# Optimization experiments

Hardware: AMD Instinct MI355X
Metric: run time of the kernel (lower is better)

The kernel has to match this reference:

```python
import jax, jax.numpy as jnp
import numpy as np

B, S, H, NH, P = 1, 2048, 1024, 16, 2
D = H // NH
SCALE = 1.0 / np.sqrt(D).astype(np.float32)


def _lin(x, W, b):
    # x: [..., in] @ W: [in, out] + b: [out]
    return x @ W + b


def _split_heads(x):
    # [..., S, H] -> [..., NH, S, D]
    return x.reshape(*x.shape[:-2], x.shape[-2], NH, D).swapaxes(-3, -2)


def _merge_heads(x):
    # [..., NH, S, D] -> [..., S, H]
    return x.swapaxes(-3, -2).reshape(*x.shape[:-3], x.shape[-2], H)


def setup_inputs() -> dict:
    key = jax.random.key(0)
    ks = jax.random.split(key, 20)
    w = lambda k, i, o: jax.random.normal(k, (i, o), jnp.float32) * 0.02
    inp = {
        "hidden_states": jax.random.normal(ks[0], (B, S, H), jnp.float32),
        "past_states": jax.random.normal(ks[1], (P, B, S, H), jnp.float32),
        "Wq": w(ks[2], H, H), "bq": jnp.zeros((H,), jnp.float32),
        "Wk": w(ks[3], H, H), "bk": jnp.zeros((H,), jnp.float32),
        "Wv": w(ks[4], H, H), "bv": jnp.zeros((H,), jnp.float32),
        "Wo": w(ks[5], H, H), "bo": jnp.zeros((H,), jnp.float32),
        "Wrq": w(ks[6], H, H), "brq": jnp.zeros((H,), jnp.float32),
        "Wrk": w(ks[7], H, H), "brk": jnp.zeros((H,), jnp.float32),
        "Wrv": w(ks[8], H, H), "brv": jnp.zeros((H,), jnp.float32),
        "Wg": w(ks[9], 2 * H, H), "bg": jnp.zeros((H,), jnp.float32),
    }
    return inp


def reference(hidden_states, past_states, Wq, bq, Wk, bk, Wv, bv, Wo, bo,
              Wrq, brq, Wrk, brk, Wrv, brv, Wg, bg):
    # --- standard self-attention ---
    q = _split_heads(_lin(hidden_states, Wq, bq))  # [B,NH,S,D]
    k = _split_heads(_lin(hidden_states, Wk, bk))
    v = _split_heads(_lin(hidden_states, Wv, bv))
    scores = jnp.einsum('bhsd,bhtd->bhst', q, k) * SCALE
    attn = jax.nn.softmax(scores, axis=-1)
    ctx = jnp.einsum('bhst,bhtd->bhsd', attn, v)
    output = _lin(_merge_heads(ctx), Wo, bo)  # [B,S,H]

    # --- recursive attention over past states (recursion_level > 0) ---
    rq = _split_heads(_lin(output, Wrq, brq))           # [B,NH,S,D]
    rk = _split_heads(_lin(past_states, Wrk, brk))      # [P,B,NH,S,D]
    rv = _split_heads(_lin(past_states, Wrv, brv))
    rscores = jnp.einsum('bhsd,pbhtd->pbhst', rq, rk) * SCALE
    rattn = jax.nn.softmax(rscores, axis=-1)
    rctx = jnp.einsum('pbhst,pbhtd->pbhsd', rattn, rv)
    recursive_output = _merge_heads(rctx).mean(axis=0)  # [B,S,H]

    gate = jax.nn.sigmoid(_lin(jnp.concatenate([output, recursive_output], axis=-1), Wg, bg))
    output = output * (1.0 - gate) + recursive_output * gate
    return output
```

## Files before the change

### kernel.cpp

```cpp
#include <hip/hip_runtime.h>
#include <hip/hip_bf16.h>

#define S_LEN 2048
#define HDIM  1024
#define NHEAD 16
#define DHEAD 64
#define SCALE_F 0.125f

typedef __bf16 bf16;
typedef __bf16 bf16x4 __attribute__((ext_vector_type(4)));
typedef __bf16 bf16x8 __attribute__((ext_vector_type(8)));
typedef float  f32x4  __attribute__((ext_vector_type(4)));

#define MFMA16(a,b,c) __builtin_amdgcn_mfma_f32_16x16x32_bf16((a),(b),(c),0,0,0)

__global__ void cvt_f32_bf16_kernel(const float* __restrict__ in,
                                    bf16* __restrict__ out, int n4) {
  int i = blockIdx.x * blockDim.x + threadIdx.x;
  int stride = gridDim.x * blockDim.x;
  for (; i < n4; i += stride) {
    float4 v = ((const float4*)in)[i];
    bf16x4 o = { (bf16)v.x, (bf16)v.y, (bf16)v.z, (bf16)v.w };
    ((bf16x4*)out)[i] = o;
  }
}

struct TrJob { const float* in; bf16* out; };
struct TrArgs { TrJob j[8]; };

__global__ void transp_cvt_kernel(TrArgs args, int rows, int cols) {
  TrJob t = args.j[blockIdx.z];
  __shared__ float tile[32][33];
  int tx = threadIdx.x, ty = threadIdx.y;
  int c0 = blockIdx.x * 32, r0 = blockIdx.y * 32;
  for (int j = ty; j < 32; j += 8)
    tile[j][tx] = t.in[(size_t)(r0 + j) * cols + c0 + tx];
  __syncthreads();
  for (int j = ty; j < 32; j += 8)
    t.out[(size_t)(c0 + j) * rows + r0 + tx] = (bf16)tile[tx][j];
}

__global__ void transp_head_kernel(const bf16* __restrict__ in,
                                   bf16* __restrict__ out) {
  __shared__ bf16 tile[32][33];
  int h = blockIdx.z;
  int t0 = blockIdx.x * 32, d0 = blockIdx.y * 32;
  int tx = threadIdx.x, ty = threadIdx.y;
  for (int j = ty; j < 32; j += 8)
    tile[j][tx] = in[(size_t)(t0 + j) * HDIM + h * DHEAD + d0 + tx];
  __syncthreads();
  for (int j = ty; j < 32; j += 8)
    out[((size_t)h * DHEAD + d0 + j) * S_LEN + t0 + tx] = tile[tx][j];
}

struct GemmJob { const bf16* A; const bf16* Bt; const float* bias; bf16* Cb; float* Cf; };
struct GemmArgs { GemmJob j[6]; };

__launch_bounds__(256)
__global__ void gemm_bt_kernel(GemmArgs args, int M, int N, int K) {
  GemmJob jb = args.j[blockIdx.z];
  const int bn = blockIdx.x, bm = blockIdx.y;
  const int tid = threadIdx.x;
  const int wave = tid >> 6, lane = tid & 63;
  const int wr = wave >> 1, wc = wave & 1;
  const int l16 = lane & 15, lq = lane >> 4;

  __shared__ alignas(16) bf16 As[128][40];
  __shared__ alignas(16) bf16 Bs[128][40];

  f32x4 acc[4][4];
#pragma unroll
  for (int i = 0; i < 4; ++i)
#pragma unroll
    for (int j = 0; j < 4; ++j) acc[i][j] = (f32x4){0.f, 0.f, 0.f, 0.f};

  const bf16* Ap = jb.A + (size_t)bm * 128 * K;
  const bf16* Bp = jb.Bt + (size_t)bn * 128 * K;

  for (int kt = 0; kt < K; kt += 32) {
    __syncthreads();
#pragma unroll
    for (int it = 0; it < 2; ++it) {
      int idx = tid + it * 256;
      int r = idx >> 2, c8 = (idx & 3) << 3;
      *(bf16x8*)(&As[r][c8]) = *(const bf16x8*)(Ap + (size_t)r * K + kt + c8);
      *(bf16x8*)(&Bs[r][c8]) = *(const bf16x8*)(Bp + (size_t)r * K + kt + c8);
    }
    __syncthreads();

    bf16x8 af[4], bfr[4];
#pragma unroll
    for (int i = 0; i < 4; ++i)
      af[i] = *(const bf16x8*)(&As[wr * 64 + i * 16 + l16][lq * 8]);
#pragma unroll
    for (int j = 0; j < 4; ++j)
      bfr[j] = *(const bf16x8*)(&Bs[wc * 64 + j * 16 + l16][lq * 8]);
#pragma unroll
    for (int i = 0; i < 4; ++i)
#pragma unroll
      for (int j = 0; j < 4; ++j)
        acc[i][j] = MFMA16(af[i], bfr[j], acc[i][j]);
  }

#pragma unroll
  for (int i = 0; i < 4; ++i) {
#pragma unroll
    for (int j = 0; j < 4; ++j) {
      int row0 = bm * 128 + wr * 64 + i * 16 + lq * 4;
      int col  = bn * 128 + wc * 64 + j * 16 + l16;
      float bv = jb.bias ? jb.bias[col] : 0.0f;
#pragma unroll
      for (int r = 0; r < 4; ++r) {
        float v = acc[i][j][r] + bv;
        size_t off = (size_t)(row0 + r) * N + col;
        if (jb.Cb) jb.Cb[off] = (bf16)v;
        if (jb.Cf) jb.Cf[off] = v;
      }
    }
  }
}

__launch_bounds__(256)
__global__ void flash_attn_kernel(const bf16* __restrict__ Q,
                                  const bf16* __restrict__ Kin,
                                  const bf16* __restrict__ VT,
                                  bf16* __restrict__ Ob,
                                  float* __restrict__ Of,
                                  size_t kStride, size_t vStride, size_t oStride) {
  const int qb = blockIdx.x, h = blockIdx.y, p = blockIdx.z;
  const bf16* Kp = Kin + (size_t)p * kStride;
  const bf16* Vp = VT + (size_t)p * vStride;
  const int tid = threadIdx.x;
  const int wave = tid >> 6, lane = tid & 63;
  const int l16 = lane & 15, lq = lane >> 4;

  __shared__ alignas(16) bf16 Ks[64][72];
  __shared__ alignas(16) bf16 Vs[64][72];
  __shared__ alignas(16) bf16 Ps[4][16][72];

  bf16x8 qf[2];
  {
    const bf16* qptr = Q + (size_t)(qb * 64 + wave * 16 + l16) * HDIM + h * DHEAD + lq * 8;
    qf[0] = *(const bf16x8*)qptr;
    qf[1] = *(const bf16x8*)(qptr + 32);
  }

  float m_run[4], l_run[4];
  f32x4 oacc[4];
#pragma unroll
  for (int r = 0; r < 4; ++r) { m_run[r] = -1e30f; l_run[r] = 0.f; }
#pragma unroll
  for (int j = 0; j < 4; ++j) oacc[j] = (f32x4){0.f, 0.f, 0.f, 0.f};

  for (int tb = 0; tb < S_LEN / 64; ++tb) {
    __syncthreads();
#pragma unroll
    for (int it = 0; it < 2; ++it) {
      int idx = tid + it * 256;
      int r = idx >> 3, c8 = (idx & 7) << 3;
      *(bf16x8*)(&Ks[r][c8]) = *(const bf16x8*)(Kp + (size_t)(tb * 64 + r) * HDIM + h * DHEAD + c8);
      *(bf16x8*)(&Vs[r][c8]) = *(const bf16x8*)(Vp + ((size_t)h * DHEAD + r) * S_LEN + tb * 64 + c8);
    }
    __syncthreads();

    f32x4 sf[4];
#pragma unroll
    for (int j = 0; j < 4; ++j) sf[j] = (f32x4){0.f, 0.f, 0.f, 0.f};
#pragma unroll
    for (int j = 0; j < 4; ++j)
#pragma unroll
      for (int kk = 0; kk < 2; ++kk) {
        bf16x8 kf = *(const bf16x8*)(&Ks[j * 16 + l16][kk * 32 + lq * 8]);
        sf[j] = MFMA16(qf[kk], kf, sf[j]);
      }

    float mx[4];
#pragma unroll
    for (int r = 0; r < 4; ++r) {
      sf[0][r] *= SCALE_F; sf[1][r] *= SCALE_F; sf[2][r] *= SCALE_F; sf[3][r] *= SCALE_F;
      mx[r] = fmaxf(fmaxf(sf[0][r], sf[1][r]), fmaxf(sf[2][r], sf[3][r]));
    }
#pragma unroll
    for (int m = 1; m < 16; m <<= 1)
#pragma unroll
      for (int r = 0; r < 4; ++r) mx[r] = fmaxf(mx[r], __shfl_xor(mx[r], m, 16));

    float corr[4], rs[4];
#pragma unroll
    for (int r = 0; r < 4; ++r) {
      float mnew = fmaxf(m_run[r], mx[r]);
      corr[r] = __expf(m_run[r] - mnew);
      m_run[r] = mnew;
      rs[r] = 0.f;
    }
#pragma unroll
    for (int j = 0; j < 4; ++j)
#pragma unroll
      for (int r = 0; r < 4; ++r) {
        float pv = __expf(sf[j][r] - m_run[r]);
        sf[j][r] = pv;
        rs[r] += pv;
      }
#pragma unroll
    for (int m = 1; m < 16; m <<= 1)
#pragma unroll
      for (int r = 0; r < 4; ++r) rs[r] += __shfl_xor(rs[r], m, 16);
#pragma unroll
    for (int r = 0; r < 4; ++r) l_run[r] = l_run[r] * corr[r] + rs[r];
#pragma unroll
    for (int j = 0; j < 4; ++j)
#pragma unroll
      for (int r = 0; r < 4; ++r) oacc[j][r] *= corr[r];

#pragma unroll
    for (int j = 0; j < 4; ++j)
#pragma unroll
      for (int r = 0; r < 4; ++r)
        Ps[wave][lq * 4 + r][j * 16 + l16] = (bf16)sf[j][r];
    __syncthreads();

    bf16x8 pf[2];
    pf[0] = *(const bf16x8*)(&Ps[wave][l16][lq * 8]);
    pf[1] = *(const bf16x8*)(&Ps[wave][l16][32 + lq * 8]);
#pragma unroll
    for (int j = 0; j < 4; ++j)
#pragma unroll
      for (int kk = 0; kk < 2; ++kk) {
        bf16x8 vf = *(const bf16x8*)(&Vs[j * 16 + l16][kk * 32 + lq * 8]);
        oacc[j] = MFMA16(pf[kk], vf, oacc[j]);
      }
  }

  float* Ofp = Of ? Of + (size_t)p * oStride : nullptr;
#pragma unroll
  for (int r = 0; r < 4; ++r) {
    float inv = 1.0f / l_run[r];
    int row = qb * 64 + wave * 16 + lq * 4 + r;
#pragma unroll
    for (int j = 0; j < 4; ++j) {
      float v = oacc[j][r] * inv;
      size_t off = (size_t)row * HDIM + h * DHEAD + j * 16 + l16;
      if (Ob)  Ob[off] = (bf16)v;
      if (Ofp) Ofp[off] = v;
    }
  }
}

__global__ void mean_gate_prep_kernel(const float* __restrict__ rc,
                                      const bf16* __restrict__ outb,
                                      float* __restrict__ rof,
                                      bf16* __restrict__ acat,
                                      int n) {
  int i = blockIdx.x * blockDim.x + threadIdx.x;
  int stride = gridDim.x * blockDim.x;
  for (; i < n; i += stride) {
    float ro = 0.5f * (rc[i] + rc[i + n]);
    rof[i] = ro;
    int srow = i >> 10, col = i & 1023;
    size_t base = (size_t)srow * 2048;
    acat[base + col] = outb[i];
    acat[base + 1024 + col] = (bf16)ro;
  }
}

__global__ void final_gate_kernel(const float* __restrict__ outf,
                                  const float* __restrict__ rof,
                                  const float* __restrict__ glog,
                                  float* __restrict__ out, int n) {
  int i = blockIdx.x * blockDim.x + threadIdx.x;
  int stride = gridDim.x * blockDim.x;
  for (; i < n; i += stride) {
    float g = 1.0f / (1.0f + __expf(-glog[i]));
    out[i] = outf[i] * (1.0f - g) + rof[i] * g;
  }
}

extern "C" void kernel_launch(void* const* d_in, const int* in_sizes, int n_in,
                              void* d_out, int out_size, void* d_ws, size_t ws_size,
                              hipStream_t stream) {
  const float* hs   = (const float*)d_in[0];
  const float* past = (const float*)d_in[1];
  const float* Wq = (const float*)d_in[2];   const float* bq = (const float*)d_in[3];
  const float* Wk = (const float*)d_in[4];   const float* bk = (const float*)d_in[5];
  const float* Wv = (const float*)d_in[6];   const float* bv = (const float*)d_in[7];
  const float* Wo = (const float*)d_in[8];   const float* bo = (const float*)d_in[9];
  const float* Wrq = (const float*)d_in[10]; const float* brq = (const float*)d_in[11];
  const float* Wrk = (const float*)d_in[12]; const float* brk = (const float*)d_in[13];
  const float* Wrv = (const float*)d_in[14]; const float* brv = (const float*)d_in[15];
  const float* Wg  = (const float*)d_in[16]; const float* bg  = (const float*)d_in[17];

  char* wp = (char*)d_ws;
  auto alloc = [&](size_t bytes) -> void* {
    void* p = (void*)wp;
    wp += (bytes + 255) & ~(size_t)255;
    return p;
  };
  const size_t NE = (size_t)S_LEN * HDIM;

  bf16* hs_b   = (bf16*)alloc(NE * 2);
  bf16* past_b = (bf16*)alloc(2 * NE * 2);
  bf16* Wqt  = (bf16*)alloc((size_t)HDIM * HDIM * 2);
  bf16* Wkt  = (bf16*)alloc((size_t)HDIM * HDIM * 2);
  bf16* Wvt  = (bf16*)alloc((size_t)HDIM * HDIM * 2);
  bf16* Wot  = (bf16*)alloc((size_t)HDIM * HDIM * 2);
  bf16* Wrqt = (bf16*)alloc((size_t)HDIM * HDIM * 2);
  bf16* Wrkt = (bf16*)alloc((size_t)HDIM * HDIM * 2);
  bf16* Wrvt = (bf16*)alloc((size_t)HDIM * HDIM * 2);
  bf16* Wgt  = (bf16*)alloc((size_t)2 * HDIM * HDIM * 2);
  bf16* q_b   = (bf16*)alloc(NE * 2);
  bf16* k_b   = (bf16*)alloc(NE * 2);
  bf16* v_b   = (bf16*)alloc(NE * 2);
  bf16* vT_b  = (bf16*)alloc(NE * 2);
  bf16* ctx_b = (bf16*)alloc(NE * 2);
  bf16* out_b = (bf16*)alloc(NE * 2);
  float* out_f = (float*)alloc(NE * 4);
  bf16* rq_b  = (bf16*)alloc(NE * 2);
  bf16* rk_b  = (bf16*)alloc(2 * NE * 2);
  bf16* rv_b  = (bf16*)alloc(2 * NE * 2);
  bf16* rvT_b = (bf16*)alloc(2 * NE * 2);
  float* rctx_f = (float*)alloc(2 * NE * 4);
  float* ro_f   = (float*)alloc(NE * 4);
  bf16* acat_b  = (bf16*)alloc(2 * NE * 2);
  float* glog_f = (float*)alloc(NE * 4);

  cvt_f32_bf16_kernel<<<2048, 256, 0, stream>>>(hs, hs_b, (int)(NE / 4));
  cvt_f32_bf16_kernel<<<2048, 256, 0, stream>>>(past, past_b, (int)(2 * NE / 4));

  TrArgs ta{};
  ta.j[0] = {Wq, Wqt};  ta.j[1] = {Wk, Wkt};  ta.j[2] = {Wv, Wvt};
  ta.j[3] = {Wo, Wot};  ta.j[4] = {Wrq, Wrqt}; ta.j[5] = {Wrk, Wrkt};
  ta.j[6] = {Wrv, Wrvt};
  transp_cvt_kernel<<<dim3(32, 32, 7), dim3(32, 8), 0, stream>>>(ta, 1024, 1024);
  TrArgs tg{};
  tg.j[0] = {Wg, Wgt};
  transp_cvt_kernel<<<dim3(32, 64, 1), dim3(32, 8), 0, stream>>>(tg, 2048, 1024);

  GemmArgs g1{};
  g1.j[0] = {hs_b, Wqt, bq, q_b, nullptr};
  g1.j[1] = {hs_b, Wkt, bk, k_b, nullptr};
  g1.j[2] = {hs_b, Wvt, bv, v_b, nullptr};
  gemm_bt_kernel<<<dim3(8, 16, 3), 256, 0, stream>>>(g1, 2048, 1024, 1024);

  transp_head_kernel<<<dim3(64, 2, 16), dim3(32, 8), 0, stream>>>(v_b, vT_b);

  flash_attn_kernel<<<dim3(32, 16, 1), 256, 0, stream>>>(
      q_b, k_b, vT_b, ctx_b, nullptr, 0, 0, 0);

  GemmArgs g2{};
  g2.j[0] = {ctx_b, Wot, bo, out_b, out_f};
  gemm_bt_kernel<<<dim3(8, 16, 1), 256, 0, stream>>>(g2, 2048, 1024, 1024);

  GemmArgs g3{};
  g3.j[0] = {out_b,        Wrqt, brq, rq_b,        nullptr};
  g3.j[1] = {past_b,       Wrkt, brk, rk_b,        nullptr};
  g3.j[2] = {past_b + NE,  Wrkt, brk, rk_b + NE,   nullptr};
  g3.j[3] = {past_b,       Wrvt, brv, rv_b,        nullptr};
  g3.j[4] = {past_b + NE,  Wrvt, brv, rv_b + NE,   nullptr};
  gemm_bt_kernel<<<dim3(8, 16, 5), 256, 0, stream>>>(g3, 2048, 1024, 1024);

  transp_head_kernel<<<dim3(64, 2, 16), dim3(32, 8), 0, stream>>>(rv_b, rvT_b);
  transp_head_kernel<<<dim3(64, 2, 16), dim3(32, 8), 0, stream>>>(rv_b + NE, rvT_b + NE);

  flash_attn_kernel<<<dim3(32, 16, 2), 256, 0, stream>>>(
      rq_b, rk_b, rvT_b, nullptr, rctx_f, NE, NE, NE);

  mean_gate_prep_kernel<<<2048, 256, 0, stream>>>(rctx_f, out_b, ro_f, acat_b, (int)NE);

  GemmArgs g4{};
  g4.j[0] = {acat_b, Wgt, bg, nullptr, glog_f};
  gemm_bt_kernel<<<dim3(8, 16, 1), 256, 0, stream>>>(g4, 2048, 1024, 2048);

  final_gate_kernel<<<2048, 256, 0, stream>>>(out_f, ro_f, glog_f, (float*)d_out, (int)NE);
}
```

Before: 504.6 us.

## Use direct global-to-LDS loads in GEMM and transposed-MFMA softmax in attention

The GEMM tile loads now use global_load_lds, so data goes from global memory straight into unpadded LDS instead of passing through registers. The attention kernel swaps the MFMA operands so each lane owns one query row. That turns the row max and sum reductions into two cross-lane shuffles, lets P be written as packed bf16x4, and drops a block-wide barrier in favour of a wave-local lgkmcnt wait. The softmax scale and log2(e) are folded into the Q projection epilogue so exp2f can replace __expf. The unpadded LDS layout may cause bank conflicts on fragment reads, and the folded scale is stored in bf16, which slightly changes Q rounding.

After: 474.6 us. 1.06x faster.

```diff
diff --git a/kernel.cpp b/kernel.cpp
--- a/kernel.cpp
+++ b/kernel.cpp
@@ -6,6 +6,7 @@
 #define NHEAD 16
 #define DHEAD 64
 #define SCALE_F 0.125f
+#define QSCALE  (0.125f * 1.44269504088896340736f)
 
 typedef __bf16 bf16;
 typedef __bf16 bf16x4 __attribute__((ext_vector_type(4)));
@@ -13,6 +14,12 @@
 typedef float  f32x4  __attribute__((ext_vector_type(4)));
 
 #define MFMA16(a,b,c) __builtin_amdgcn_mfma_f32_16x16x32_bf16((a),(b),(c),0,0,0)
+
+__device__ __forceinline__ void gload16(const bf16* g, bf16* lds_wave_base) {
+  __builtin_amdgcn_global_load_lds(
+      (const __attribute__((address_space(1))) void*)g,
+      (__attribute__((address_space(3))) void*)lds_wave_base, 16, 0, 0);
+}
 
 __global__ void cvt_f32_bf16_kernel(const float* __restrict__ in,
                                     bf16* __restrict__ out, int n4) {
@@ -53,7 +60,7 @@
     out[((size_t)h * DHEAD + d0 + j) * S_LEN + t0 + tx] = tile[tx][j];
 }
 
-struct GemmJob { const bf16* A; const bf16* Bt; const float* bias; bf16* Cb; float* Cf; };
+struct GemmJob { const bf16* A; const bf16* Bt; const float* bias; bf16* Cb; float* Cf; float cscale; };
 struct GemmArgs { GemmJob j[6]; };
 
 __launch_bounds__(256)
@@ -65,8 +72,8 @@
   const int wr = wave >> 1, wc = wave & 1;
   const int l16 = lane & 15, lq = lane >> 4;
 
-  __shared__ alignas(16) bf16 As[128][40];
-  __shared__ alignas(16) bf16 Bs[128][40];
+  __shared__ alignas(16) bf16 As[128 * 32];
+  __shared__ alignas(16) bf16 Bs[128 * 32];
 
   f32x4 acc[4][4];
 #pragma unroll
@@ -77,24 +84,28 @@
   const bf16* Ap = jb.A + (size_t)bm * 128 * K;
   const bf16* Bp = jb.Bt + (size_t)bn * 128 * K;
 
+  const int r0 = tid >> 2,           c0 = (tid & 3) << 3;
+  const int r1 = (tid + 256) >> 2,   c1 = ((tid + 256) & 3) << 3;
+  bf16* ldsA0 = As + wave * 512;
+  bf16* ldsA1 = As + 2048 + wave * 512;
+  bf16* ldsB0 = Bs + wave * 512;
+  bf16* ldsB1 = Bs + 2048 + wave * 512;
+
   for (int kt = 0; kt < K; kt += 32) {
     __syncthreads();
-#pragma unroll
-    for (int it = 0; it < 2; ++it) {
-      int idx = tid + it * 256;
-      int r = idx >> 2, c8 = (idx & 3) << 3;
-      *(bf16x8*)(&As[r][c8]) = *(const bf16x8*)(Ap + (size_t)r * K + kt + c8);
-      *(bf16x8*)(&Bs[r][c8]) = *(const bf16x8*)(Bp + (size_t)r * K + kt + c8);
-    }
+    gload16(Ap + (size_t)r0 * K + kt + c0, ldsA0);
+    gload16(Ap + (size_t)r1 * K + kt + c1, ldsA1);
+    gload16(Bp + (size_t)r0 * K + kt + c0, ldsB0);
+    gload16(Bp + (size_t)r1 * K + kt + c1, ldsB1);
     __syncthreads();
 
     bf16x8 af[4], bfr[4];
 #pragma unroll
     for (int i = 0; i < 4; ++i)
-      af[i] = *(const bf16x8*)(&As[wr * 64 + i * 16 + l16][lq * 8]);
-#pragma unroll
-    for (int j = 0; j < 4; ++j)
-      bfr[j] = *(const bf16x8*)(&Bs[wc * 64 + j * 16 + l16][lq * 8]);
+      af[i] = *(const bf16x8*)(As + (size_t)(wr * 64 + i * 16 + l16) * 32 + lq * 8);
+#pragma unroll
+    for (int j = 0; j < 4; ++j)
+      bfr[j] = *(const bf16x8*)(Bs + (size_t)(wc * 64 + j * 16 + l16) * 32 + lq * 8);
 #pragma unroll
     for (int i = 0; i < 4; ++i)
 #pragma unroll
@@ -111,7 +122,7 @@
       float bv = jb.bias ? jb.bias[col] : 0.0f;
 #pragma unroll
       for (int r = 0; r < 4; ++r) {
-        float v = acc[i][j][r] + bv;
+        float v = (acc[i][j][r] + bv) * jb.cscale;
         size_t off = (size_t)(row0 + r) * N + col;
         if (jb.Cb) jb.Cb[off] = (bf16)v;
         if (jb.Cf) jb.Cf[off] = v;
@@ -145,10 +156,8 @@
     qf[1] = *(const bf16x8*)(qptr + 32);
   }
 
-  float m_run[4], l_run[4];
+  float m_run = -1e30f, l_run = 0.f;
   f32x4 oacc[4];
-#pragma unroll
-  for (int r = 0; r < 4; ++r) { m_run[r] = -1e30f; l_run[r] = 0.f; }
 #pragma unroll
   for (int j = 0; j < 4; ++j) oacc[j] = (f32x4){0.f, 0.f, 0.f, 0.f};
 
@@ -171,53 +180,44 @@
 #pragma unroll
       for (int kk = 0; kk < 2; ++kk) {
         bf16x8 kf = *(const bf16x8*)(&Ks[j * 16 + l16][kk * 32 + lq * 8]);
-        sf[j] = MFMA16(qf[kk], kf, sf[j]);
+        sf[j] = MFMA16(kf, qf[kk], sf[j]);
       }
 
-    float mx[4];
-#pragma unroll
-    for (int r = 0; r < 4; ++r) {
-      sf[0][r] *= SCALE_F; sf[1][r] *= SCALE_F; sf[2][r] *= SCALE_F; sf[3][r] *= SCALE_F;
-      mx[r] = fmaxf(fmaxf(sf[0][r], sf[1][r]), fmaxf(sf[2][r], sf[3][r]));
-    }
-#pragma unroll
-    for (int m = 1; m < 16; m <<= 1)
-#pragma unroll
-      for (int r = 0; r < 4; ++r) mx[r] = fmaxf(mx[r], __shfl_xor(mx[r], m, 16));
-
-    float corr[4], rs[4];
-#pragma unroll
-    for (int r = 0; r < 4; ++r) {
-      float mnew = fmaxf(m_run[r], mx[r]);
-      corr[r] = __expf(m_run[r] - mnew);
-      m_run[r] = mnew;
-      rs[r] = 0.f;
-    }
+    float mx = -1e30f;
+#pragma unroll
+    for (int j = 0; j < 4; ++j)
+#pragma unroll
+      for (int r = 0; r < 4; ++r) mx = fmaxf(mx, sf[j][r]);
+    mx = fmaxf(mx, __shfl_xor(mx, 16));
+    mx = fmaxf(mx, __shfl_xor(mx, 32));
+
+    float mnew = fmaxf(m_run, mx);
+    float corr = exp2f(m_run - mnew);
+    m_run = mnew;
+
+    float rs = 0.f;
 #pragma unroll
     for (int j = 0; j < 4; ++j)
 #pragma unroll
       for (int r = 0; r < 4; ++r) {
-        float pv = __expf(sf[j][r] - m_run[r]);
+        float pv = exp2f(sf[j][r] - mnew);
         sf[j][r] = pv;
-        rs[r] += pv;
+        rs += pv;
       }
-#pragma unroll
-    for (int m = 1; m < 16; m <<= 1)
-#pragma unroll
-      for (int r = 0; r < 4; ++r) rs[r] += __shfl_xor(rs[r], m, 16);
-#pragma unroll
-    for (int r = 0; r < 4; ++r) l_run[r] = l_run[r] * corr[r] + rs[r];
-#pragma unroll
-    for (int j = 0; j < 4; ++j)
-#pragma unroll
-      for (int r = 0; r < 4; ++r) oacc[j][r] *= corr[r];
-
-#pragma unroll
-    for (int j = 0; j < 4; ++j)
-#pragma unroll
-      for (int r = 0; r < 4; ++r)
-        Ps[wave][lq * 4 + r][j * 16 + l16] = (bf16)sf[j][r];
-    __syncthreads();
+    rs += __shfl_xor(rs, 16);
+    rs += __shfl_xor(rs, 32);
+    l_run = l_run * corr + rs;
+#pragma unroll
+    for (int j = 0; j < 4; ++j) {
+      oacc[j][0] *= corr; oacc[j][1] *= corr; oacc[j][2] *= corr; oacc[j][3] *= corr;
+    }
+
+#pragma unroll
+    for (int j = 0; j < 4; ++j) {
+      bf16x4 pk = { (bf16)sf[j][0], (bf16)sf[j][1], (bf16)sf[j][2], (bf16)sf[j][3] };
+      *(bf16x4*)(&Ps[wave][l16][j * 16 + lq * 4]) = pk;
+    }
+    asm volatile("s_waitcnt lgkmcnt(0)" ::: "memory");
 
     bf16x8 pf[2];
     pf[0] = *(const bf16x8*)(&Ps[wave][l16][lq * 8]);
@@ -226,22 +226,25 @@
     for (int j = 0; j < 4; ++j)
 #pragma unroll
       for (int kk = 0; kk < 2; ++kk) {
-        bf16x8 vf = *(const bf16x8*)(&Vs[j * 16 + l16][kk * 32 + lq * 8]);
-        oacc[j] = MFMA16(pf[kk], vf, oacc[j]);
+        bf16x8 vtf = *(const bf16x8*)(&Vs[j * 16 + l16][kk * 32 + lq * 8]);
+        oacc[j] = MFMA16(vtf, pf[kk], oacc[j]);
       }
   }
 
-  float* Ofp = Of ? Of + (size_t)p * oStride : nullptr;
-#pragma unroll
-  for (int r = 0; r < 4; ++r) {
-    float inv = 1.0f / l_run[r];
-    int row = qb * 64 + wave * 16 + lq * 4 + r;
-#pragma unroll
-    for (int j = 0; j < 4; ++j) {
-      float v = oacc[j][r] * inv;
-      size_t off = (size_t)row * HDIM + h * DHEAD + j * 16 + l16;
-      if (Ob)  Ob[off] = (bf16)v;
-      if (Ofp) Ofp[off] = v;
+  const float inv = 1.0f / l_run;
+  const int q = qb * 64 + wave * 16 + l16;
+#pragma unroll
+  for (int j = 0; j < 4; ++j) {
+    size_t off = (size_t)q * HDIM + h * DHEAD + j * 16 + lq * 4;
+    float o0 = oacc[j][0] * inv, o1 = oacc[j][1] * inv,
+          o2 = oacc[j][2] * inv, o3 = oacc[j][3] * inv;
+    if (Ob) {
+      bf16x4 ov = { (bf16)o0, (bf16)o1, (bf16)o2, (bf16)o3 };
+      *(bf16x4*)(Ob + off) = ov;
+    }
+    if (Of) {
+      float4 ov = { o0, o1, o2, o3 };
+      *(float4*)(Of + (size_t)p * oStride + off) = ov;
     }
   }
 }
@@ -336,9 +339,9 @@
   transp_cvt_kernel<<<dim3(32, 64, 1), dim3(32, 8), 0, stream>>>(tg, 2048, 1024);
 
   GemmArgs g1{};
-  g1.j[0] = {hs_b, Wqt, bq, q_b, nullptr};
-  g1.j[1] = {hs_b, Wkt, bk, k_b, nullptr};
-  g1.j[2] = {hs_b, Wvt, bv, v_b, nullptr};
+  g1.j[0] = {hs_b, Wqt, bq, q_b, nullptr, QSCALE};
+  g1.j[1] = {hs_b, Wkt, bk, k_b, nullptr, 1.0f};
+  g1.j[2] = {hs_b, Wvt, bv, v_b, nullptr, 1.0f};
   gemm_bt_kernel<<<dim3(8, 16, 3), 256, 0, stream>>>(g1, 2048, 1024, 1024);
 
   transp_head_kernel<<<dim3(64, 2, 16), dim3(32, 8), 0, stream>>>(v_b, vT_b);
@@ -347,15 +350,15 @@
       q_b, k_b, vT_b, ctx_b, nullptr, 0, 0, 0);
 
   GemmArgs g2{};
-  g2.j[0] = {ctx_b, Wot, bo, out_b, out_f};
+  g2.j[0] = {ctx_b, Wot, bo, out_b, out_f, 1.0f};
   gemm_bt_kernel<<<dim3(8, 16, 1), 256, 0, stream>>>(g2, 2048, 1024, 1024);
 
   GemmArgs g3{};
-  g3.j[0] = {out_b,        Wrqt, brq, rq_b,        nullptr};
-  g3.j[1] = {past_b,       Wrkt, brk, rk_b,        nullptr};
-  g3.j[2] = {past_b + NE,  Wrkt, brk, rk_b + NE,   nullptr};
-  g3.j[3] = {past_b,       Wrvt, brv, rv_b,        nullptr};
-  g3.j[4] = {past_b + NE,  Wrvt, brv, rv_b + NE,   nullptr};
+  g3.j[0] = {out_b,        Wrqt, brq, rq_b,      nullptr, QSCALE};
+  g3.j[1] = {past_b,       Wrkt, brk, rk_b,      nullptr, 1.0f};
+  g3.j[2] = {past_b + NE,  Wrkt, brk, rk_b + NE, nullptr, 1.0f};
+  g3.j[3] = {past_b,       Wrvt, brv, rv_b,      nullptr, 1.0f};
+  g3.j[4] = {past_b + NE,  Wrvt, brv, rv_b + NE, nullptr, 1.0f};
   gemm_bt_kernel<<<dim3(8, 16, 5), 256, 0, stream>>>(g3, 2048, 1024, 1024);
 
   transp_head_kernel<<<dim3(64, 2, 16), dim3(32, 8), 0, stream>>>(rv_b, rvT_b);
@@ -367,7 +370,7 @@
   mean_gate_prep_kernel<<<2048, 256, 0, stream>>>(rctx_f, out_b, ro_f, acat_b, (int)NE);
 
   GemmArgs g4{};
-  g4.j[0] = {acat_b, Wgt, bg, nullptr, glog_f};
+  g4.j[0] = {acat_b, Wgt, bg, nullptr, glog_f, 1.0f};
   gemm_bt_kernel<<<dim3(8, 16, 1), 256, 0, stream>>>(g4, 2048, 1024, 2048);
 
   final_gate_kernel<<<2048, 256, 0, stream>>>(out_f, ro_f, glog_f, (float*)d_out, (int)NE);
```
